# Performance work log

Hardware: AMD Instinct MI355X
Metric: run time of the kernel (lower is better)

## Reference

```python
import jax, jax.numpy as jnp
import numpy as np

TEMPERATURE = 0.1
NORMALIZE = True


def setup_inputs() -> dict:
    key = jax.random.key(0)
    k1, k2 = jax.random.split(key)
    B, D = 4096, 512
    return {
        "z_i": jax.random.normal(k1, (B, D), dtype=jnp.float32),
        "z_j": jax.random.normal(k2, (B, D), dtype=jnp.float32),
    }


def _l2norm(x):
    return x / jnp.sqrt(jnp.sum(x * x, axis=-1, keepdims=True))


def reference(z_i, z_j):
    if NORMALIZE:
        z_i = _l2norm(z_i)
        z_j = _l2norm(z_j)
    B = z_i.shape[0]

    inv_t = 1.0 / TEMPERATURE
    logits_aa = (z_i @ z_i.T) * inv_t  # [B, B]
    logits_bb = (z_j @ z_j.T) * inv_t
    logits_ab = (z_i @ z_j.T) * inv_t
    logits_ba = (z_j @ z_i.T) * inv_t

    # Static off-diagonal column indices: row i keeps cols 0..B-1 except i,
    # in ascending order (matches torch boolean-mask row-major extraction).
    j = jnp.arange(B - 1)[None, :]
    i = jnp.arange(B)[:, None]
    idx = j + (j >= i)  # [B, B-1] int32

    take = lambda m: jnp.take_along_axis(m, idx, axis=1)  # [B, B-1]

    pos = jnp.concatenate([jnp.diagonal(logits_ab), jnp.diagonal(logits_ba)])[:, None]  # [2B, 1]
    neg_a = jnp.concatenate([take(logits_aa), take(logits_ab)], axis=1)  # [B, 2(B-1)]
    neg_b = jnp.concatenate([take(logits_ba), take(logits_bb)], axis=1)
    neg = jnp.concatenate([neg_a, neg_b], axis=0)  # [2B, 2(B-1)]

    logits = jnp.concatenate([pos, neg], axis=1)  # [2B, 2B-1]
    logp = jax.nn.log_softmax(logits, axis=1)
    # Original forward uses labels = torch.ones(2B).long() -> target class 1.
    loss = -jnp.mean(logp[:, 1])
    return loss
```

## Files before the change

kernel.cpp:

```cpp
#include <hip/hip_runtime.h>
#include <hip/hip_bf16.h>
#include <hip/hip_fp8.h>


#define BB 4096
#define DD 512
#define NN 8192
#define TILE 128
#define KB 128
#define NBLK 2080

typedef __attribute__((ext_vector_type(4))) float f32x4;

#define AS1 __attribute__((address_space(1)))
#define AS3 __attribute__((address_space(3)))
static __device__ __forceinline__ void gload_lds16(const void* g, void* l) {
    __builtin_amdgcn_global_load_lds((const AS1 void*)g, (AS3 void*)l, 16, 0, 0);
}

__global__ __launch_bounds__(256)
void normalize_kernel(const float* __restrict__ zi, const float* __restrict__ zj,
                      unsigned char* __restrict__ M, float* __restrict__ rowsum) {
    const int wave = threadIdx.x >> 6;
    const int lane = threadIdx.x & 63;
    const int row  = blockIdx.x * 4 + wave;
    if (threadIdx.x < 4) rowsum[blockIdx.x * 4 + threadIdx.x] = 0.f;
    const float* src = (row < BB) ? (zi + (size_t)row * DD)
                                  : (zj + (size_t)(row - BB) * DD);
    float4 v0 = ((const float4*)src)[lane * 2 + 0];
    float4 v1 = ((const float4*)src)[lane * 2 + 1];
    float ss = v0.x*v0.x + v0.y*v0.y + v0.z*v0.z + v0.w*v0.w
             + v1.x*v1.x + v1.y*v1.y + v1.z*v1.z + v1.w*v1.w;
    #pragma unroll
    for (int off = 1; off <= 32; off <<= 1) ss += __shfl_xor(ss, off);
    const float inv = rsqrtf(ss);
    const float vals[8] = {v0.x*inv, v0.y*inv, v0.z*inv, v0.w*inv,
                           v1.x*inv, v1.y*inv, v1.z*inv, v1.w*inv};
    union { long u; unsigned char b[8]; } pk;
    #pragma unroll
    for (int j = 0; j < 8; ++j)
        pk.b[j] = __hip_cvt_float_to_fp8(vals[j], __HIP_SATFINITE, __HIP_E4M3);
    ((long*)(M + (size_t)row * DD))[lane] = pk.u;
}

__global__ __launch_bounds__(256, 4)
void gram_lse_kernel(const unsigned char* __restrict__ Mg,
                     float* __restrict__ rowsum, float* __restrict__ targets) {
    __shared__ __align__(16) char As[TILE * KB];
    __shared__ __align__(16) char Bs[TILE * KB];

    const int d = blockIdx.x;
    const int p = (d & 7) * 260 + (d >> 3);
    int by = (int)((sqrtf(8.0f * (float)p + 1.0f) - 1.0f) * 0.5f);
    while ((by + 1) * (by + 2) / 2 <= p) ++by;
    while (by * (by + 1) / 2 > p) --by;
    const int bx = p - by * (by + 1) / 2;

    const int rowBase = bx * TILE;
    const int colBase = by * TILE;
    const bool diag = (bx == by);
    const int tid  = threadIdx.x;
    const int wave = tid >> 6;
    const int lane = tid & 63;
    const int wr = (wave >> 1) * 64;
    const int wc = (wave & 1) * 64;
    const int l15 = lane & 15;
    const int l4  = lane >> 4;

    const int sg  = (tid & 7) ^ ((tid >> 3) & 7);
    const int sr0 = tid >> 3;
    const unsigned char* gA0 = Mg + (size_t)(rowBase + sr0) * DD + sg * 16;
    const unsigned char* gB0 = Mg + (size_t)(colBase + sr0) * DD + sg * 16;
    char* lA0 = As + tid * 16;
    char* lB0 = Bs + tid * 16;

    const int r7 = l15 & 7;
    const int qh = l4 >> 1, ql = l4 & 1;
    const int aoff0 = (wr + l15) * KB + ql * 8;
    const int boff0 = (wc + l15) * KB + ql * 8;
    const char* BsP = diag ? As : Bs;

    f32x4 acc[4][4] = {};

    for (int k0 = 0; k0 < DD; k0 += KB) {
        __syncthreads();
        #pragma unroll
        for (int i = 0; i < 4; ++i)
            gload_lds16(gA0 + k0 + (size_t)i * 32 * DD, lA0 + i * 4096);
        if (!diag) {
            #pragma unroll
            for (int i = 0; i < 4; ++i)
                gload_lds16(gB0 + k0 + (size_t)i * 32 * DD, lB0 + i * 4096);
        }
        __syncthreads();
        #pragma unroll
        for (int ks = 0; ks < 4; ++ks) {
            const int so = ((((ks << 1) | qh) ^ r7) << 4);
            long a[4], b[4];
            #pragma unroll
            for (int mi = 0; mi < 4; ++mi)
                a[mi] = *(const long*)(As + aoff0 + mi * 2048 + so);
            #pragma unroll
            for (int ni = 0; ni < 4; ++ni)
                b[ni] = *(const long*)(BsP + boff0 + ni * 2048 + so);
            #pragma unroll
            for (int mi = 0; mi < 4; ++mi)
                #pragma unroll
                for (int ni = 0; ni < 4; ++ni)
                    acc[mi][ni] = __builtin_amdgcn_mfma_f32_16x16x32_fp8_fp8(
                        a[mi], b[ni], acc[mi][ni], 0, 0, 0);
        }
    }

    float cs[4] = {0.f, 0.f, 0.f, 0.f};
    #pragma unroll
    for (int mi = 0; mi < 4; ++mi) {
        float rs[4] = {0.f, 0.f, 0.f, 0.f};
        #pragma unroll
        for (int ni = 0; ni < 4; ++ni) {
            const int gcol = colBase + wc + ni * 16 + l15;
            #pragma unroll
            for (int r = 0; r < 4; ++r) {
                const int grow = rowBase + wr + mi * 16 + l4 * 4 + r;
                float logit = 10.f * acc[mi][ni][r];
                float e = __expf(logit - 10.f);
                if (grow == gcol) e = 0.f;
                rs[r] += e;
                cs[ni] += e;
                if (rowBase == 0 && grow < 2) {
                    const int j0 = ((gcol & (BB - 1)) == 0) ? 1 : 0;
                    if (grow == j0) targets[gcol] = logit;
                }
            }
        }
        #pragma unroll
        for (int m = 1; m <= 8; m <<= 1)
            #pragma unroll
            for (int r = 0; r < 4; ++r)
                rs[r] += __shfl_xor(rs[r], m);
        if (l15 == 0) {
            #pragma unroll
            for (int r = 0; r < 4; ++r)
                atomicAdd(&rowsum[rowBase + wr + mi * 16 + l4 * 4 + r], rs[r]);
        }
    }
    if (!diag) {
        #pragma unroll
        for (int ni = 0; ni < 4; ++ni) {
            cs[ni] += __shfl_xor(cs[ni], 16);
            cs[ni] += __shfl_xor(cs[ni], 32);
        }
        if (l4 == 0) {
            #pragma unroll
            for (int ni = 0; ni < 4; ++ni)
                atomicAdd(&rowsum[colBase + wc + ni * 16 + l15], cs[ni]);
        }
    }
}

__global__ __launch_bounds__(1024)
void finalize_kernel(const float* __restrict__ rowsum,
                     const float* __restrict__ targets, float* __restrict__ out) {
    const int tid = threadIdx.x;
    float s = 0.f;
    #pragma unroll
    for (int t = tid; t < NN; t += 1024)
        s += targets[t] - 10.f - __logf(rowsum[t]);
    #pragma unroll
    for (int off = 1; off <= 32; off <<= 1) s += __shfl_xor(s, off);
    __shared__ float red[16];
    if ((tid & 63) == 0) red[tid >> 6] = s;
    __syncthreads();
    if (tid == 0) {
        float t = 0.f;
        #pragma unroll
        for (int i = 0; i < 16; ++i) t += red[i];
        out[0] = -t / (float)NN;
    }
}

extern "C" void kernel_launch(void* const* d_in, const int* in_sizes, int n_in,
                              void* d_out, int out_size, void* d_ws, size_t ws_size,
                              hipStream_t stream) {
    const float* zi = (const float*)d_in[0];
    const float* zj = (const float*)d_in[1];

    unsigned char* M = (unsigned char*)d_ws;
    float* rowsum  = (float*)((char*)d_ws + (size_t)NN * DD);
    float* targets = rowsum + NN;
    float* out = (float*)d_out;

    normalize_kernel<<<NN / 4, 256, 0, stream>>>(zi, zj, M, rowsum);
    gram_lse_kernel<<<NBLK, 256, 0, stream>>>(M, rowsum, targets);
    finalize_kernel<<<1, 1024, 0, stream>>>(rowsum, targets, out);
}
```

Measured before the change: 100.7 us.

## Switch Gram tile MFMA to 32x32x64 scaled fp8 instruction

New measurement: 108.3 us. 1.08x slower.

```diff
diff --git a/kernel.cpp b/kernel.cpp
--- a/kernel.cpp
+++ b/kernel.cpp
@@ -10,7 +10,9 @@
 #define KB 128
 #define NBLK 2080
 
-typedef __attribute__((ext_vector_type(4))) float f32x4;
+typedef __attribute__((ext_vector_type(4)))  int   int4v;
+typedef __attribute__((ext_vector_type(8)))  int   int8v;
+typedef __attribute__((ext_vector_type(16))) float f32x16;
 
 #define AS1 __attribute__((address_space(1)))
 #define AS3 __attribute__((address_space(3)))
@@ -43,7 +45,7 @@
     ((long*)(M + (size_t)row * DD))[lane] = pk.u;
 }
 
-__global__ __launch_bounds__(256, 4)
+__global__ __launch_bounds__(256, 3)
 void gram_lse_kernel(const unsigned char* __restrict__ Mg,
                      float* __restrict__ rowsum, float* __restrict__ targets) {
     __shared__ __align__(16) char As[TILE * KB];
@@ -64,8 +66,9 @@
     const int lane = tid & 63;
     const int wr = (wave >> 1) * 64;
     const int wc = (wave & 1) * 64;
-    const int l15 = lane & 15;
-    const int l4  = lane >> 4;
+    const int l31 = lane & 31;
+    const int hi2 = lane >> 5;
+    const int r7  = l31 & 7;
 
     const int sg  = (tid & 7) ^ ((tid >> 3) & 7);
     const int sr0 = tid >> 3;
@@ -74,13 +77,11 @@
     char* lA0 = As + tid * 16;
     char* lB0 = Bs + tid * 16;
 
-    const int r7 = l15 & 7;
-    const int qh = l4 >> 1, ql = l4 & 1;
-    const int aoff0 = (wr + l15) * KB + ql * 8;
-    const int boff0 = (wc + l15) * KB + ql * 8;
+    const int arow0 = (wr + l31) * KB;
+    const int brow0 = (wc + l31) * KB;
     const char* BsP = diag ? As : Bs;
 
-    f32x4 acc[4][4] = {};
+    f32x16 acc[2][2] = {};
 
     for (int k0 = 0; k0 < DD; k0 += KB) {
         __syncthreads();
@@ -94,34 +95,45 @@
         }
         __syncthreads();
         #pragma unroll
-        for (int ks = 0; ks < 4; ++ks) {
-            const int so = ((((ks << 1) | qh) ^ r7) << 4);
-            long a[4], b[4];
-            #pragma unroll
-            for (int mi = 0; mi < 4; ++mi)
-                a[mi] = *(const long*)(As + aoff0 + mi * 2048 + so);
-            #pragma unroll
-            for (int ni = 0; ni < 4; ++ni)
-                b[ni] = *(const long*)(BsP + boff0 + ni * 2048 + so);
-            #pragma unroll
-            for (int mi = 0; mi < 4; ++mi)
+        for (int ks = 0; ks < 2; ++ks) {
+            const int gb = ks * 4 + hi2 * 2;
+            int8v a[2], b[2];
+            #pragma unroll
+            for (int mi = 0; mi < 2; ++mi) {
+                int4v lo = *(const int4v*)(As + arow0 + mi * 4096 + (((gb + 0) ^ r7) << 4));
+                int4v hi = *(const int4v*)(As + arow0 + mi * 4096 + (((gb + 1) ^ r7) << 4));
+                a[mi] = __builtin_shufflevector(lo, hi, 0, 1, 2, 3, 4, 5, 6, 7);
+            }
+            #pragma unroll
+            for (int ni = 0; ni < 2; ++ni) {
+                int4v lo = *(const int4v*)(BsP + brow0 + ni * 4096 + (((gb + 0) ^ r7) << 4));
+                int4v hi = *(const int4v*)(BsP + brow0 + ni * 4096 + (((gb + 1) ^ r7) << 4));
+                b[ni] = __builtin_shufflevector(lo, hi, 0, 1, 2, 3, 4, 5, 6, 7);
+            }
+            #pragma unroll
+            for (int mi = 0; mi < 2; ++mi)
                 #pragma unroll
-                for (int ni = 0; ni < 4; ++ni)
-                    acc[mi][ni] = __builtin_amdgcn_mfma_f32_16x16x32_fp8_fp8(
-                        a[mi], b[ni], acc[mi][ni], 0, 0, 0);
-        }
-    }
-
-    float cs[4] = {0.f, 0.f, 0.f, 0.f};
-    #pragma unroll
-    for (int mi = 0; mi < 4; ++mi) {
-        float rs[4] = {0.f, 0.f, 0.f, 0.f};
-        #pragma unroll
-        for (int ni = 0; ni < 4; ++ni) {
-            const int gcol = colBase + wc + ni * 16 + l15;
-            #pragma unroll
-            for (int r = 0; r < 4; ++r) {
-                const int grow = rowBase + wr + mi * 16 + l4 * 4 + r;
+                for (int ni = 0; ni < 2; ++ni)
+                    acc[mi][ni] = __builtin_amdgcn_mfma_scale_f32_32x32x64_f8f6f4(
+                        a[mi], b[ni], acc[mi][ni],
+                        0, 0,
+                        0, 127,
+                        0, 127);
+        }
+    }
+
+    float cs[2] = {0.f, 0.f};
+    #pragma unroll
+    for (int mi = 0; mi < 2; ++mi) {
+        float rs[16];
+        #pragma unroll
+        for (int r = 0; r < 16; ++r) rs[r] = 0.f;
+        #pragma unroll
+        for (int ni = 0; ni < 2; ++ni) {
+            const int gcol = colBase + wc + ni * 32 + l31;
+            #pragma unroll
+            for (int r = 0; r < 16; ++r) {
+                const int grow = rowBase + wr + mi * 32 + (r & 3) + 8 * (r >> 2) + 4 * hi2;
                 float logit = 10.f * acc[mi][ni][r];
                 float e = __expf(logit - 10.f);
                 if (grow == gcol) e = 0.f;
@@ -134,26 +146,23 @@
             }
         }
         #pragma unroll
-        for (int m = 1; m <= 8; m <<= 1)
-            #pragma unroll
-            for (int r = 0; r < 4; ++r)
+        for (int m = 1; m <= 16; m <<= 1)
+            #pragma unroll
+            for (int r = 0; r < 16; ++r)
                 rs[r] += __shfl_xor(rs[r], m);
-        if (l15 == 0) {
-            #pragma unroll
-            for (int r = 0; r < 4; ++r)
-                atomicAdd(&rowsum[rowBase + wr + mi * 16 + l4 * 4 + r], rs[r]);
+        if (l31 == 0) {
+            #pragma unroll
+            for (int r = 0; r < 16; ++r)
+                atomicAdd(&rowsum[rowBase + wr + mi * 32 + (r & 3) + 8 * (r >> 2) + 4 * hi2],
+                          rs[r]);
         }
     }
     if (!diag) {
         #pragma unroll
-        for (int ni = 0; ni < 4; ++ni) {
-            cs[ni] += __shfl_xor(cs[ni], 16);
+        for (int ni = 0; ni < 2; ++ni) {
             cs[ni] += __shfl_xor(cs[ni], 32);
-        }
-        if (l4 == 0) {
-            #pragma unroll
-            for (int ni = 0; ni < 4; ++ni)
-                atomicAdd(&rowsum[colBase + wc + ni * 16 + l15], cs[ni]);
+            if (hi2 == 0)
+                atomicAdd(&rowsum[colBase + wc + ni * 32 + l31], cs[ni]);
         }
     }
 }
```

## Switch fp8 Gram to 16x16x128 scaled MFMA with permuted K layout

Applied to the files above, without the earlier changes.

Measured after the change: 211.7 us. +110.1%, slower.

```diff
diff --git a/kernel.cpp b/kernel.cpp
--- a/kernel.cpp
+++ b/kernel.cpp
@@ -10,6 +10,7 @@
 #define KB 128
 #define NBLK 2080
 
+typedef __attribute__((ext_vector_type(8))) int   int8v;
 typedef __attribute__((ext_vector_type(4))) float f32x4;
 
 #define AS1 __attribute__((address_space(1)))
@@ -40,10 +41,11 @@
     #pragma unroll
     for (int j = 0; j < 8; ++j)
         pk.b[j] = __hip_cvt_float_to_fp8(vals[j], __HIP_SATFINITE, __HIP_E4M3);
-    ((long*)(M + (size_t)row * DD))[lane] = pk.u;
-}
-
-__global__ __launch_bounds__(256, 4)
+    const int swp = (row >> 3) & 1;
+    ((long*)(M + (size_t)row * DD))[lane ^ swp] = pk.u;
+}
+
+__global__ __launch_bounds__(256, 3)
 void gram_lse_kernel(const unsigned char* __restrict__ Mg,
                      float* __restrict__ rowsum, float* __restrict__ targets) {
     __shared__ __align__(16) char As[TILE * KB];
@@ -66,6 +68,8 @@
     const int wc = (wave & 1) * 64;
     const int l15 = lane & 15;
     const int l4  = lane >> 4;
+    const int r7  = l15 & 7;
+    const int r3  = (l15 >> 3) & 1;
 
     const int sg  = (tid & 7) ^ ((tid >> 3) & 7);
     const int sr0 = tid >> 3;
@@ -74,10 +78,10 @@
     char* lA0 = As + tid * 16;
     char* lB0 = Bs + tid * 16;
 
-    const int r7 = l15 & 7;
-    const int qh = l4 >> 1, ql = l4 & 1;
-    const int aoff0 = (wr + l15) * KB + ql * 8;
-    const int boff0 = (wc + l15) * KB + ql * 8;
+    const int g0off = (((2 * l4 + 0) ^ r7) << 4) | (r3 << 3);
+    const int g1off = (((2 * l4 + 1) ^ r7) << 4) | (r3 << 3);
+    const int arow0 = (wr + l15) * KB;
+    const int brow0 = (wc + l15) * KB;
     const char* BsP = diag ? As : Bs;
 
     f32x4 acc[4][4] = {};
@@ -93,24 +97,39 @@
                 gload_lds16(gB0 + k0 + (size_t)i * 32 * DD, lB0 + i * 4096);
         }
         __syncthreads();
-        #pragma unroll
-        for (int ks = 0; ks < 4; ++ks) {
-            const int so = ((((ks << 1) | qh) ^ r7) << 4);
-            long a[4], b[4];
-            #pragma unroll
-            for (int mi = 0; mi < 4; ++mi)
-                a[mi] = *(const long*)(As + aoff0 + mi * 2048 + so);
+
+        int8v a[4], b[4];
+        #pragma unroll
+        for (int mi = 0; mi < 4; ++mi) {
+            union { long l[4]; int8v v; } u;
+            const char* base = As + arow0 + mi * 2048;
+            u.l[0] = *(const long*)(base + g0off);
+            u.l[1] = *(const long*)(base + (g0off ^ 8));
+            u.l[2] = *(const long*)(base + g1off);
+            u.l[3] = *(const long*)(base + (g1off ^ 8));
+            a[mi] = u.v;
+        }
+        #pragma unroll
+        for (int ni = 0; ni < 4; ++ni) {
+            union { long l[4]; int8v v; } u;
+            const char* base = BsP + brow0 + ni * 2048;
+            u.l[0] = *(const long*)(base + g0off);
+            u.l[1] = *(const long*)(base + (g0off ^ 8));
+            u.l[2] = *(const long*)(base + g1off);
+            u.l[3] = *(const long*)(base + (g1off ^ 8));
+            b[ni] = u.v;
+        }
+        #pragma unroll
+        for (int mi = 0; mi < 4; ++mi)
             #pragma unroll
             for (int ni = 0; ni < 4; ++ni)
-                b[ni] = *(const long*)(BsP + boff0 + ni * 2048 + so);
-            #pragma unroll
-            for (int mi = 0; mi < 4; ++mi)
-                #pragma unroll
-                for (int ni = 0; ni < 4; ++ni)
-                    acc[mi][ni] = __builtin_amdgcn_mfma_f32_16x16x32_fp8_fp8(
-                        a[mi], b[ni], acc[mi][ni], 0, 0, 0);
-        }
-    }
+                acc[mi][ni] = __builtin_amdgcn_mfma_scale_f32_16x16x128_f8f6f4(
+                    a[mi], b[ni], acc[mi][ni],
+                    0, 0,
+                    0, 127,
+                    0, 127);
+    }
+
 
     float cs[4] = {0.f, 0.f, 0.f, 0.f};
     #pragma unroll
```

## Double-buffer LDS tiles with smaller K chunks to overlap loads and MFMA

Applied to the files above, without the earlier changes.

Result: slower. 142.6 us (+41.6%).

```diff
diff --git a/kernel.cpp b/kernel.cpp
--- a/kernel.cpp
+++ b/kernel.cpp
@@ -7,7 +7,7 @@
 #define DD 512
 #define NN 8192
 #define TILE 128
-#define KB 128
+#define KB 64
 #define NBLK 2080
 
 typedef __attribute__((ext_vector_type(4))) float f32x4;
@@ -46,8 +46,8 @@
 __global__ __launch_bounds__(256, 4)
 void gram_lse_kernel(const unsigned char* __restrict__ Mg,
                      float* __restrict__ rowsum, float* __restrict__ targets) {
-    __shared__ __align__(16) char As[TILE * KB];
-    __shared__ __align__(16) char Bs[TILE * KB];
+    __shared__ __align__(16) char As[2][TILE * KB];
+    __shared__ __align__(16) char Bs[2][TILE * KB];
 
     const int d = blockIdx.x;
     const int p = (d & 7) * 260 + (d >> 3);
@@ -66,50 +66,73 @@
     const int wc = (wave & 1) * 64;
     const int l15 = lane & 15;
     const int l4  = lane >> 4;
-
-    const int sg  = (tid & 7) ^ ((tid >> 3) & 7);
-    const int sr0 = tid >> 3;
-    const unsigned char* gA0 = Mg + (size_t)(rowBase + sr0) * DD + sg * 16;
-    const unsigned char* gB0 = Mg + (size_t)(colBase + sr0) * DD + sg * 16;
-    char* lA0 = As + tid * 16;
-    char* lB0 = Bs + tid * 16;
-
-    const int r7 = l15 & 7;
+    const int r3b = l15 & 3;
     const int qh = l4 >> 1, ql = l4 & 1;
-    const int aoff0 = (wr + l15) * KB + ql * 8;
-    const int boff0 = (wc + l15) * KB + ql * 8;
-    const char* BsP = diag ? As : Bs;
+
+    const int sg  = ((tid & 3) ^ ((tid >> 2) & 3)) * 16;
+    const int sr  = tid >> 2;
+    const unsigned char* gA = Mg + (size_t)(rowBase + sr) * DD + sg;
+    const unsigned char* gB = Mg + (size_t)(colBase + sr) * DD + sg;
+    const int ldst = tid * 16;
+
+    const int so0 = (((0 + qh) ^ r3b) << 4) | (ql << 3);
+    const int so1 = (((2 + qh) ^ r3b) << 4) | (ql << 3);
+    const int arow = (wr + l15) * KB;
+    const int brow = (wc + l15) * KB;
 
     f32x4 acc[4][4] = {};
 
-    for (int k0 = 0; k0 < DD; k0 += KB) {
+    #pragma unroll
+    for (int i = 0; i < 2; ++i)
+        gload_lds16(gA + (size_t)i * 64 * DD, &As[0][ldst + i * 4096]);
+    if (!diag) {
+        #pragma unroll
+        for (int i = 0; i < 2; ++i)
+            gload_lds16(gB + (size_t)i * 64 * DD, &Bs[0][ldst + i * 4096]);
+    }
+    __syncthreads();
+
+    for (int c = 0; c < 8; ++c) {
+        const int cur = c & 1, nxt = cur ^ 1;
+        const char* Ab = As[cur];
+        const char* Bb = diag ? As[cur] : Bs[cur];
+
+        long a0[4], a1[4], b0[4], b1[4];
+        #pragma unroll
+        for (int mi = 0; mi < 4; ++mi) {
+            a0[mi] = *(const long*)(Ab + arow + mi * 1024 + so0);
+            a1[mi] = *(const long*)(Ab + arow + mi * 1024 + so1);
+        }
+        #pragma unroll
+        for (int ni = 0; ni < 4; ++ni) {
+            b0[ni] = *(const long*)(Bb + brow + ni * 1024 + so0);
+            b1[ni] = *(const long*)(Bb + brow + ni * 1024 + so1);
+        }
+
+        if (c < 7) {
+            const unsigned char* pA = gA + (c + 1) * KB;
+            #pragma unroll
+            for (int i = 0; i < 2; ++i)
+                gload_lds16(pA + (size_t)i * 64 * DD, &As[nxt][ldst + i * 4096]);
+            if (!diag) {
+                const unsigned char* pB = gB + (c + 1) * KB;
+                #pragma unroll
+                for (int i = 0; i < 2; ++i)
+                    gload_lds16(pB + (size_t)i * 64 * DD, &Bs[nxt][ldst + i * 4096]);
+            }
+        }
+
+        #pragma unroll
+        for (int mi = 0; mi < 4; ++mi)
+            #pragma unroll
+            for (int ni = 0; ni < 4; ++ni) {
+                acc[mi][ni] = __builtin_amdgcn_mfma_f32_16x16x32_fp8_fp8(
+                    a0[mi], b0[ni], acc[mi][ni], 0, 0, 0);
+                acc[mi][ni] = __builtin_amdgcn_mfma_f32_16x16x32_fp8_fp8(
+                    a1[mi], b1[ni], acc[mi][ni], 0, 0, 0);
+            }
+
         __syncthreads();
-        #pragma unroll
-        for (int i = 0; i < 4; ++i)
-            gload_lds16(gA0 + k0 + (size_t)i * 32 * DD, lA0 + i * 4096);
-        if (!diag) {
-            #pragma unroll
-            for (int i = 0; i < 4; ++i)
-                gload_lds16(gB0 + k0 + (size_t)i * 32 * DD, lB0 + i * 4096);
-        }
-        __syncthreads();
-        #pragma unroll
-        for (int ks = 0; ks < 4; ++ks) {
-            const int so = ((((ks << 1) | qh) ^ r7) << 4);
-            long a[4], b[4];
-            #pragma unroll
-            for (int mi = 0; mi < 4; ++mi)
-                a[mi] = *(const long*)(As + aoff0 + mi * 2048 + so);
-            #pragma unroll
-            for (int ni = 0; ni < 4; ++ni)
-                b[ni] = *(const long*)(BsP + boff0 + ni * 2048 + so);
-            #pragma unroll
-            for (int mi = 0; mi < 4; ++mi)
-                #pragma unroll
-                for (int ni = 0; ni < 4; ++ni)
-                    acc[mi][ni] = __builtin_amdgcn_mfma_f32_16x16x32_fp8_fp8(
-                        a[mi], b[ni], acc[mi][ni], 0, 0, 0);
-        }
     }
 
     float cs[4] = {0.f, 0.f, 0.f, 0.f};
```
